# Kernel optimization log

Hardware: AMD Instinct MI355X
Metric: run time of the kernel (lower is better)

Reference implementation:

```python
import jax, jax.numpy as jnp
import numpy as np

HIDDEN = 1024
HEADS = 16
HEAD_DIM = HIDDEN // HEADS
RANK = 256
B, S = 4, 2048


def setup_inputs() -> dict:
    key = jax.random.key(0)
    ks = jax.random.split(key, 10)
    sc_in = 1.0 / np.sqrt(HIDDEN)
    sc_r = 1.0 / np.sqrt(RANK)
    inp = {"hidden_states": jax.random.normal(ks[0], (B, S, HIDDEN), dtype=jnp.float32)}
    names = ["q", "k", "v"]
    for i, n in enumerate(names):
        inp[f"{n}A"] = jax.random.normal(ks[1 + 3 * i], (HIDDEN, RANK), dtype=jnp.float32) * sc_in
        inp[f"{n}B"] = jax.random.normal(ks[2 + 3 * i], (RANK, HIDDEN), dtype=jnp.float32) * sc_r
        inp[f"{n}b"] = jnp.zeros((HIDDEN,), dtype=jnp.float32)
    return inp


def _split_heads(x):
    # [B,S,H*D] -> [B,H,S,D]
    Bh, Sh, _ = x.shape
    return x.reshape(Bh, Sh, HEADS, HEAD_DIM).transpose(0, 2, 1, 3)


def reference(hidden_states, qA, qB, qb, kA, kB, kb, vA, vB, vb):
    # Low-rank projections: x @ A @ B + b (factorized linear)
    q = hidden_states @ qA @ qB + qb
    k = hidden_states @ kA @ kB + kb
    v = hidden_states @ vA @ vB + vb
    q = _split_heads(q)  # [B,H,S,D]
    k = _split_heads(k)
    v = _split_heads(v)
    scores = jnp.einsum("bhqd,bhkd->bhqk", q, k) / np.sqrt(HEAD_DIM)
    probs = jax.nn.softmax(scores, axis=-1)  # dropout is identity at inference
    ctx = jnp.einsum("bhqk,bhkd->bhqd", probs, v)
    ctx = ctx.transpose(0, 2, 1, 3).reshape(hidden_states.shape[0], hidden_states.shape[1], HIDDEN)
    return ctx
```

## Files before the change

kernel.cpp:

```cpp
#include <hip/hip_runtime.h>


typedef unsigned short u16;
typedef unsigned int   u32;
typedef __attribute__((ext_vector_type(4)))  float    f32x4;
typedef __attribute__((ext_vector_type(16))) float    f32x16;
typedef __attribute__((ext_vector_type(8)))  short    short8;
typedef __attribute__((ext_vector_type(8)))  _Float16 half8;
typedef __attribute__((ext_vector_type(4)))  u16      u16x4;

#define HID 1024
#define R_  256
#define S_  2048
#define B_  4
#define H_  16
#define D_  64
#define M_  (B_ * S_)

#define BM 128
#define BN 64
#define BK 64

#define KVB 64
#define NT  (S_ / KVB)
#define SCL 0.18033688011112f
#define MSHIFT 8.0f

__device__ __forceinline__ u16 f2h(float f) {
    _Float16 h = (_Float16)f;
    return __builtin_bit_cast(u16, h);
}
__device__ __forceinline__ u32 pkrtz(float a, float b) {
    auto r = __builtin_amdgcn_cvt_pkrtz(a, b);
    return __builtin_bit_cast(u32, r);
}

__device__ __forceinline__ f32x4 mfma16(short8 a, short8 b, f32x4 c) {
    return __builtin_amdgcn_mfma_f32_16x16x32_f16(
        __builtin_bit_cast(half8, a), __builtin_bit_cast(half8, b), c, 0, 0, 0);
}
__device__ __forceinline__ f32x16 mfma32(short8 a, short8 b, f32x16 c) {
    return __builtin_amdgcn_mfma_f32_32x32x16_f16(
        __builtin_bit_cast(half8, a), __builtin_bit_cast(half8, b), c, 0, 0, 0);
}

__device__ __forceinline__ void gload16(const u16* g, u16* l) {
    __builtin_amdgcn_global_load_lds(
        (__attribute__((address_space(1))) const void*)g,
        (__attribute__((address_space(3))) void*)l,
        16, 0, 0);
}

#if defined(__has_builtin)
#if __has_builtin(__builtin_amdgcn_permlane32_swap)
#define HAVE_PLSWAP 1
#endif
#endif
__device__ __forceinline__ void plswap(u32 x, u32 y, u32& lo, u32& hi) {
#ifdef HAVE_PLSWAP
    typedef __attribute__((ext_vector_type(2))) unsigned uv2;
    uv2 r = __builtin_amdgcn_permlane32_swap(x, y, false, false);
    lo = r.x; hi = r.y;
#else
    u32 ty = (u32)__shfl_xor((int)y, 32);
    u32 tx = (u32)__shfl_xor((int)x, 32);
    int h = (threadIdx.x & 63) >> 5;
    lo = h ? ty : x;
    hi = h ? y : tx;
#endif
}

__global__ __launch_bounds__(256) void prep_kernel(
    const float* __restrict__ hs, u16* __restrict__ hsb,
    const float* __restrict__ qA, const float* __restrict__ kA, const float* __restrict__ vA,
    const float* __restrict__ qB, const float* __restrict__ kB, const float* __restrict__ vB,
    u16* __restrict__ At, u16* __restrict__ Bt) {
    int bx = blockIdx.x;
    if (bx < 8192) {
        int i = (bx * 256 + threadIdx.x) * 4;
        float4 v = *(const float4*)(hs + i);
        u16x4 u;
        u[0] = f2h(v.x); u[1] = f2h(v.y); u[2] = f2h(v.z); u[3] = f2h(v.w);
        *(u16x4*)(hsb + i) = u;
        return;
    }
    int pb = bx - 8192;
    int which = pb >> 10;
    int o = (pb & 1023) * 256 + threadIdx.x;
    if (which < 3) {
        const float* src = (which == 0) ? qA : (which == 1) ? kA : vA;
        u16* dst = At + (size_t)which * R_ * HID;
        int c = o >> 10, r = o & 1023;
        dst[o] = f2h(src[(size_t)r * R_ + c]);
    } else {
        int w = which - 3;
        const float* src = (w == 0) ? qB : (w == 1) ? kB : vB;
        float scl = (w == 0) ? SCL : 1.0f;
        u16* dst = Bt + (size_t)w * HID * R_;
        int c = o >> 8, r = o & 255;
        dst[o] = f2h(src[(size_t)r * HID + c] * scl);
    }
}

template <int KDIM, int NOUT, bool QKV_OUT>
__global__ __launch_bounds__(256, 3) void gemm_kernel(
    const u16* __restrict__ X, const u16* __restrict__ Wt, u16* __restrict__ Y,
    u16* __restrict__ Yv,
    const float* __restrict__ bq, const float* __restrict__ bk, const float* __restrict__ bv) {
    const int w  = blockIdx.z;
    const int m0 = blockIdx.x * BM;
    const int n0 = blockIdx.y * BN;
    const u16* Xp = X + (QKV_OUT ? (size_t)w * M_ * KDIM : (size_t)0);
    const u16* Wp = Wt + (size_t)w * NOUT * KDIM;
    u16* Yp = Y + (size_t)w * M_ * NOUT;
    const float* bias = nullptr;
    float bscl = 1.0f;
    if constexpr (QKV_OUT) { bias = (w == 0) ? bq : (w == 1) ? bk : bv; bscl = (w == 0) ? SCL : 1.0f; }

    __shared__ __align__(16) u16 As[2][BM * BK];
    __shared__ __align__(16) u16 Bs[2][BN * BK];

    const int tid  = threadIdx.x;
    const int lane = tid & 63, wv = tid >> 6;
    const int l16 = lane & 15, lg = lane >> 4;
    const int wrow = (wv >> 1) * 64, wcol = (wv & 1) * 32;

    const int sr = lane >> 3, sp = lane & 7, sc = sp ^ sr;

#define G_STAGE(bf, k0)                                                       \
    {                                                                         \
        _Pragma("unroll")                                                     \
        for (int j = 0; j < 4; ++j) {                                         \
            int ra = wv * 32 + j * 8;                                         \
            gload16(Xp + (size_t)(m0 + ra + sr) * KDIM + (k0) + sc * 8,       \
                    &As[bf][ra * 64]);                                        \
        }                                                                     \
        _Pragma("unroll")                                                     \
        for (int j = 0; j < 2; ++j) {                                         \
            int rb = wv * 16 + j * 8;                                         \
            gload16(Wp + (size_t)(n0 + rb + sr) * KDIM + (k0) + sc * 8,       \
                    &Bs[bf][rb * 64]);                                        \
        }                                                                     \
    }

    f32x4 acc[4][2];
#pragma unroll
    for (int i = 0; i < 4; ++i)
#pragma unroll
        for (int j = 0; j < 2; ++j) acc[i][j] = (f32x4){0.f, 0.f, 0.f, 0.f};

    G_STAGE(0, 0);
    int cur = 0;
    for (int k0 = 0; k0 < KDIM; k0 += BK) {
        __syncthreads();
        if (k0 + BK < KDIM) G_STAGE(cur ^ 1, k0 + BK);
        const u16* ab = &As[cur][0];
        const u16* bb = &Bs[cur][0];
#pragma unroll
        for (int ks = 0; ks < 2; ++ks) {
            short8 af[4], bf[2];
#pragma unroll
            for (int ri = 0; ri < 4; ++ri) {
                int r = wrow + ri * 16 + l16;
                int c = ks * 4 + lg;
                af[ri] = *(const short8*)(ab + r * 64 + ((c ^ (r & 7)) * 8));
            }
#pragma unroll
            for (int ci = 0; ci < 2; ++ci) {
                int r = wcol + ci * 16 + l16;
                int c = ks * 4 + lg;
                bf[ci] = *(const short8*)(bb + r * 64 + ((c ^ (r & 7)) * 8));
            }
#pragma unroll
            for (int ri = 0; ri < 4; ++ri)
#pragma unroll
                for (int ci = 0; ci < 2; ++ci)
                    acc[ri][ci] = mfma16(af[ri], bf[ci], acc[ri][ci]);
        }
        cur ^= 1;
    }
#undef G_STAGE

    if constexpr (QKV_OUT) {
        if (w == 2) {
            const int bq_ = m0 >> 11;
            const int s_base = (m0 & 2047) + wrow + lg * 4;
#pragma unroll
            for (int ci = 0; ci < 2; ++ci) {
                int c = n0 + wcol + ci * 16 + l16;
                int h = c >> 6, d = c & 63;
                u16* colp = Yv + (((size_t)(bq_ * 16 + h) * 64 + d) << 11);
                float bi = bias[c];
#pragma unroll
                for (int ri = 0; ri < 4; ++ri)
#pragma unroll
                    for (int i = 0; i < 4; ++i)
                        colp[s_base + ri * 16 + i] = f2h(acc[ri][ci][i] + bi);
            }
            return;
        }
    }
#pragma unroll
    for (int ri = 0; ri < 4; ++ri)
#pragma unroll
        for (int ci = 0; ci < 2; ++ci)
#pragma unroll
            for (int i = 0; i < 4; ++i) {
                int r = m0 + wrow + ri * 16 + lg * 4 + i;
                int c = n0 + wcol + ci * 16 + l16;
                float val = acc[ri][ci][i];
                if constexpr (QKV_OUT) val += bias[c] * bscl;
                Yp[(size_t)r * NOUT + c] = f2h(val);
            }
}

__global__ __launch_bounds__(256) void attn_kernel(
    const u16* __restrict__ Q, const u16* __restrict__ K,
    const u16* __restrict__ VT, float* __restrict__ out) {
    const int f = blockIdx.x;
    const int xcd = f & 7, idx = f >> 3;
    const int bh = xcd * 8 + (idx >> 4);
    const int qt = idx & 15;
    const int b = bh >> 4, h = bh & 15;
    const int tid = threadIdx.x, lane = tid & 63, wv = tid >> 6;
    const int l31 = lane & 31, hi = lane >> 5;
    const int q0 = qt * 128 + wv * 32;
    const int rx = l31 & 7;

    __shared__ __align__(16) u16 Ks[2][KVB * 64];
    __shared__ __align__(16) u16 Vs[2][KVB * 64];

    short8 qf[4];
    {
        const u16* qp = Q + ((size_t)(b * S_ + q0 + l31)) * HID + h * D_ + 8 * hi;
#pragma unroll
        for (int ks = 0; ks < 4; ++ks) qf[ks] = *(const short8*)(qp + 16 * ks);
    }

    f32x16 ctx0, ctx1;
#pragma unroll
    for (int i = 0; i < 16; ++i) { ctx0[i] = 0.f; ctx1[i] = 0.f; }
    float la0 = 0.f, la1 = 0.f, la2 = 0.f, la3 = 0.f;

    const int r0p = tid >> 3, pos0 = tid & 7;
    const int rA = r0p, rB = r0p + 32;
    const int slA = pos0 ^ (rA & 7), slB = pos0 ^ (rB & 7);
    const size_t kofA = (size_t)rA * HID + slA * 8, kofB = (size_t)rB * HID + slB * 8;
    const size_t vofA = (size_t)rA * S_ + slA * 8,  vofB = (size_t)rB * S_ + slB * 8;
    const int wofA = rA * 64 + pos0 * 8, wofB = rB * 64 + pos0 * 8;

    const u16* Kcur = K + (size_t)(b * S_) * HID + h * D_;
    const u16* Vcur = VT + (size_t)bh * D_ * S_;

    short8 kst0, kst1, vst0, vst1;
    kst0 = *(const short8*)(Kcur + kofA);
    kst1 = *(const short8*)(Kcur + kofB);
    vst0 = *(const short8*)(Vcur + vofA);
    vst1 = *(const short8*)(Vcur + vofB);
    *(short8*)&Ks[0][wofA] = kst0;
    *(short8*)&Ks[0][wofB] = kst1;
    *(short8*)&Vs[0][wofA] = vst0;
    *(short8*)&Vs[0][wofB] = vst1;
    __syncthreads();

    for (int t = 0; t < NT; ++t) {
        const int buf = t & 1;
        if (t + 1 < NT) {
            const u16* Kn = Kcur + (size_t)(t + 1) * KVB * HID;
            const u16* Vn = Vcur + (size_t)(t + 1) * KVB;
            kst0 = *(const short8*)(Kn + kofA);
            kst1 = *(const short8*)(Kn + kofB);
            vst0 = *(const short8*)(Vn + vofA);
            vst1 = *(const short8*)(Vn + vofB);
        }

        f32x16 p0, p1;
#pragma unroll
        for (int i = 0; i < 16; ++i) { p0[i] = -MSHIFT; p1[i] = -MSHIFT; }
        const u16* kb = &Ks[buf][0];
#pragma unroll
        for (int ks = 0; ks < 4; ++ks) {
            int sl = (2 * ks + hi) ^ rx;
            short8 a0 = *(const short8*)(kb + l31 * 64 + sl * 8);
            short8 a1 = *(const short8*)(kb + (32 + l31) * 64 + sl * 8);
            p0 = mfma32(a0, qf[ks], p0);
            p1 = mfma32(a1, qf[ks], p1);
        }

#pragma unroll
        for (int i = 0; i < 16; ++i) {
            p0[i] = __builtin_amdgcn_exp2f(p0[i]);
            p1[i] = __builtin_amdgcn_exp2f(p1[i]);
        }
#pragma unroll
        for (int i = 0; i < 4; ++i) {
            la0 += p0[i] + p0[4 + i];
            la1 += p0[8 + i] + p0[12 + i];
            la2 += p1[i] + p1[4 + i];
            la3 += p1[8 + i] + p1[12 + i];
        }

        short8 pa[4];
#define PACK_CHUNK(pv, base, dst)                                   \
        {                                                           \
            u32 x0 = pkrtz(pv[base + 0], pv[base + 1]);             \
            u32 x1 = pkrtz(pv[base + 2], pv[base + 3]);             \
            u32 x2 = pkrtz(pv[base + 4], pv[base + 5]);             \
            u32 x3 = pkrtz(pv[base + 6], pv[base + 7]);             \
            u32 w0, w1, w2, w3;                                     \
            plswap(x0, x2, w0, w2);                                 \
            plswap(x1, x3, w1, w3);                                 \
            union { u32 w[4]; short8 v; } uu;                       \
            uu.w[0] = w0; uu.w[1] = w1; uu.w[2] = w2; uu.w[3] = w3; \
            dst = uu.v;                                             \
        }
        PACK_CHUNK(p0, 0, pa[0]);
        PACK_CHUNK(p0, 8, pa[1]);
        PACK_CHUNK(p1, 0, pa[2]);
        PACK_CHUNK(p1, 8, pa[3]);
#undef PACK_CHUNK

        const u16* vb = &Vs[buf][0];
#pragma unroll
        for (int c = 0; c < 4; ++c) {
            int sl = (2 * c + hi) ^ rx;
            short8 v0 = *(const short8*)(vb + l31 * 64 + sl * 8);
            short8 v1 = *(const short8*)(vb + (32 + l31) * 64 + sl * 8);
            ctx0 = mfma32(v0, pa[c], ctx0);
            ctx1 = mfma32(v1, pa[c], ctx1);
        }

        __syncthreads();
        if (t + 1 < NT) {
            const int nb = 1 - buf;
            *(short8*)&Ks[nb][wofA] = kst0;
            *(short8*)&Ks[nb][wofB] = kst1;
            *(short8*)&Vs[nb][wofA] = vst0;
            *(short8*)&Vs[nb][wofB] = vst1;
        }
        __syncthreads();
    }

    float l = (la0 + la1) + (la2 + la3);
    l += __shfl_xor(l, 32);
    float invl = 1.0f / l;
    float* op = out + ((size_t)(b * S_ + q0 + l31)) * HID + h * D_;
#pragma unroll
    for (int g = 0; g < 4; ++g) {
        f32x4 o0, o1;
#pragma unroll
        for (int i = 0; i < 4; ++i) {
            o0[i] = ctx0[4 * g + i] * invl;
            o1[i] = ctx1[4 * g + i] * invl;
        }
        *(f32x4*)(op + 8 * g + 4 * hi) = o0;
        *(f32x4*)(op + 32 + 8 * g + 4 * hi) = o1;
    }
}

extern "C" void kernel_launch(void* const* d_in, const int* in_sizes, int n_in,
                              void* d_out, int out_size, void* d_ws, size_t ws_size,
                              hipStream_t stream) {
    const float* hs = (const float*)d_in[0];
    const float* qA = (const float*)d_in[1];
    const float* qB = (const float*)d_in[2];
    const float* qb = (const float*)d_in[3];
    const float* kA = (const float*)d_in[4];
    const float* kB = (const float*)d_in[5];
    const float* kb = (const float*)d_in[6];
    const float* vA = (const float*)d_in[7];
    const float* vB = (const float*)d_in[8];
    const float* vb = (const float*)d_in[9];

    char* ws = (char*)d_ws;
    size_t off = 0;
    u16* hsb = (u16*)(ws + off); off += (size_t)M_ * HID * 2;
    u16* At  = (u16*)(ws + off); off += (size_t)3 * R_ * HID * 2;
    u16* Bt  = (u16*)(ws + off); off += (size_t)3 * HID * R_ * 2;
    u16* T   = (u16*)(ws + off); off += (size_t)3 * M_ * R_ * 2;
    u16* QKV = (u16*)(ws + off); off += (size_t)3 * M_ * HID * 2;
    u16* VT  = (u16*)(ws + off);

    prep_kernel<<<dim3(8192 + 6144), 256, 0, stream>>>(hs, hsb, qA, kA, vA, qB, kB, vB, At, Bt);

    gemm_kernel<HID, R_, false><<<dim3(M_ / BM, R_ / BN, 3), 256, 0, stream>>>(
        hsb, At, T, nullptr, nullptr, nullptr, nullptr);
    gemm_kernel<R_, HID, true><<<dim3(M_ / BM, HID / BN, 3), 256, 0, stream>>>(
        T, Bt, QKV, VT, qb, kb, vb);

    attn_kernel<<<dim3(1024), 256, 0, stream>>>(
        QKV, QKV + (size_t)M_ * HID, VT, (float*)d_out);
}
```

Measured before the change: 150.7 us.

## Process 64 query rows per wave in attention to double K/V tile reuse

Each attention wave now handles two 32-row query sub-blocks instead of one, so every K and V fragment loaded from shared memory feeds twice as many MFMAs. The block covers 256 queries and the grid is halved to 512 blocks, which halves total K/V global and LDS traffic per query. The score accumulator is seeded from a preinitialised register vector, and launch bounds are raised to request two blocks per CU. The cost is higher register pressure from four context and four score accumulators, and fewer blocks to spread across the device.

```diff
diff --git a/kernel.cpp b/kernel.cpp
--- a/kernel.cpp
+++ b/kernel.cpp
@@ -214,33 +214,43 @@
             }
 }
 
-__global__ __launch_bounds__(256) void attn_kernel(
+__global__ __launch_bounds__(256, 2) void attn_kernel(
     const u16* __restrict__ Q, const u16* __restrict__ K,
     const u16* __restrict__ VT, float* __restrict__ out) {
     const int f = blockIdx.x;
     const int xcd = f & 7, idx = f >> 3;
-    const int bh = xcd * 8 + (idx >> 4);
-    const int qt = idx & 15;
+    const int bh = xcd * 8 + (idx >> 3);
+    const int qt = idx & 7;
     const int b = bh >> 4, h = bh & 15;
     const int tid = threadIdx.x, lane = tid & 63, wv = tid >> 6;
     const int l31 = lane & 31, hi = lane >> 5;
-    const int q0 = qt * 128 + wv * 32;
+    const int q0 = qt * 256 + wv * 64;
     const int rx = l31 & 7;
 
     __shared__ __align__(16) u16 Ks[2][KVB * 64];
     __shared__ __align__(16) u16 Vs[2][KVB * 64];
 
-    short8 qf[4];
+    short8 qf0[4], qf1[4];
     {
         const u16* qp = Q + ((size_t)(b * S_ + q0 + l31)) * HID + h * D_ + 8 * hi;
-#pragma unroll
-        for (int ks = 0; ks < 4; ++ks) qf[ks] = *(const short8*)(qp + 16 * ks);
-    }
-
-    f32x16 ctx0, ctx1;
-#pragma unroll
-    for (int i = 0; i < 16; ++i) { ctx0[i] = 0.f; ctx1[i] = 0.f; }
+        const u16* qp1 = qp + 32 * HID;
+#pragma unroll
+        for (int ks = 0; ks < 4; ++ks) {
+            qf0[ks] = *(const short8*)(qp + 16 * ks);
+            qf1[ks] = *(const short8*)(qp1 + 16 * ks);
+        }
+    }
+
+    f32x16 ctx00, ctx01, ctx10, ctx11;
+#pragma unroll
+    for (int i = 0; i < 16; ++i) { ctx00[i] = 0.f; ctx01[i] = 0.f; ctx10[i] = 0.f; ctx11[i] = 0.f; }
     float la0 = 0.f, la1 = 0.f, la2 = 0.f, la3 = 0.f;
+    float lb0 = 0.f, lb1 = 0.f, lb2 = 0.f, lb3 = 0.f;
+
+    f32x16 minit;
+#pragma unroll
+    for (int i = 0; i < 16; ++i) minit[i] = -MSHIFT;
+    asm volatile("" : "+v"(minit));
 
     const int r0p = tid >> 3, pos0 = tid & 7;
     const int rA = r0p, rB = r0p + 32;
@@ -274,33 +284,46 @@
             vst1 = *(const short8*)(Vn + vofB);
         }
 
-        f32x16 p0, p1;
-#pragma unroll
-        for (int i = 0; i < 16; ++i) { p0[i] = -MSHIFT; p1[i] = -MSHIFT; }
+        f32x16 p00, p01, p10, p11;
         const u16* kb = &Ks[buf][0];
 #pragma unroll
         for (int ks = 0; ks < 4; ++ks) {
             int sl = (2 * ks + hi) ^ rx;
             short8 a0 = *(const short8*)(kb + l31 * 64 + sl * 8);
             short8 a1 = *(const short8*)(kb + (32 + l31) * 64 + sl * 8);
-            p0 = mfma32(a0, qf[ks], p0);
-            p1 = mfma32(a1, qf[ks], p1);
+            if (ks == 0) {
+                p00 = mfma32(a0, qf0[0], minit);
+                p01 = mfma32(a1, qf0[0], minit);
+                p10 = mfma32(a0, qf1[0], minit);
+                p11 = mfma32(a1, qf1[0], minit);
+            } else {
+                p00 = mfma32(a0, qf0[ks], p00);
+                p01 = mfma32(a1, qf0[ks], p01);
+                p10 = mfma32(a0, qf1[ks], p10);
+                p11 = mfma32(a1, qf1[ks], p11);
+            }
         }
 
 #pragma unroll
         for (int i = 0; i < 16; ++i) {
-            p0[i] = __builtin_amdgcn_exp2f(p0[i]);
-            p1[i] = __builtin_amdgcn_exp2f(p1[i]);
+            p00[i] = __builtin_amdgcn_exp2f(p00[i]);
+            p01[i] = __builtin_amdgcn_exp2f(p01[i]);
+            p10[i] = __builtin_amdgcn_exp2f(p10[i]);
+            p11[i] = __builtin_amdgcn_exp2f(p11[i]);
         }
 #pragma unroll
         for (int i = 0; i < 4; ++i) {
-            la0 += p0[i] + p0[4 + i];
-            la1 += p0[8 + i] + p0[12 + i];
-            la2 += p1[i] + p1[4 + i];
-            la3 += p1[8 + i] + p1[12 + i];
-        }
-
-        short8 pa[4];
+            la0 += p00[i] + p00[4 + i];
+            la1 += p00[8 + i] + p00[12 + i];
+            la2 += p01[i] + p01[4 + i];
+            la3 += p01[8 + i] + p01[12 + i];
+            lb0 += p10[i] + p10[4 + i];
+            lb1 += p10[8 + i] + p10[12 + i];
+            lb2 += p11[i] + p11[4 + i];
+            lb3 += p11[8 + i] + p11[12 + i];
+        }
+
+        short8 pa0[4], pa1[4];
 #define PACK_CHUNK(pv, base, dst)                                   \
         {                                                           \
             u32 x0 = pkrtz(pv[base + 0], pv[base + 1]);             \
@@ -314,10 +337,14 @@
             uu.w[0] = w0; uu.w[1] = w1; uu.w[2] = w2; uu.w[3] = w3; \
             dst = uu.v;                                             \
         }
-        PACK_CHUNK(p0, 0, pa[0]);
-        PACK_CHUNK(p0, 8, pa[1]);
-        PACK_CHUNK(p1, 0, pa[2]);
-        PACK_CHUNK(p1, 8, pa[3]);
+        PACK_CHUNK(p00, 0, pa0[0]);
+        PACK_CHUNK(p00, 8, pa0[1]);
+        PACK_CHUNK(p01, 0, pa0[2]);
+        PACK_CHUNK(p01, 8, pa0[3]);
+        PACK_CHUNK(p10, 0, pa1[0]);
+        PACK_CHUNK(p10, 8, pa1[1]);
+        PACK_CHUNK(p11, 0, pa1[2]);
+        PACK_CHUNK(p11, 8, pa1[3]);
 #undef PACK_CHUNK
 
         const u16* vb = &Vs[buf][0];
@@ -326,8 +353,10 @@
             int sl = (2 * c + hi) ^ rx;
             short8 v0 = *(const short8*)(vb + l31 * 64 + sl * 8);
             short8 v1 = *(const short8*)(vb + (32 + l31) * 64 + sl * 8);
-            ctx0 = mfma32(v0, pa[c], ctx0);
-            ctx1 = mfma32(v1, pa[c], ctx1);
+            ctx00 = mfma32(v0, pa0[c], ctx00);
+            ctx01 = mfma32(v1, pa0[c], ctx01);
+            ctx10 = mfma32(v0, pa1[c], ctx10);
+            ctx11 = mfma32(v1, pa1[c], ctx11);
         }
 
         __syncthreads();
@@ -341,20 +370,27 @@
         __syncthreads();
     }
 
-    float l = (la0 + la1) + (la2 + la3);
-    l += __shfl_xor(l, 32);
-    float invl = 1.0f / l;
-    float* op = out + ((size_t)(b * S_ + q0 + l31)) * HID + h * D_;
+    float l0 = (la0 + la1) + (la2 + la3);
+    l0 += __shfl_xor(l0, 32);
+    float l1 = (lb0 + lb1) + (lb2 + lb3);
+    l1 += __shfl_xor(l1, 32);
+    float invl0 = 1.0f / l0, invl1 = 1.0f / l1;
+    float* op0 = out + ((size_t)(b * S_ + q0 + l31)) * HID + h * D_;
+    float* op1 = op0 + (size_t)32 * HID;
 #pragma unroll
     for (int g = 0; g < 4; ++g) {
-        f32x4 o0, o1;
+        f32x4 o00, o01, o10, o11;
 #pragma unroll
         for (int i = 0; i < 4; ++i) {
-            o0[i] = ctx0[4 * g + i] * invl;
-            o1[i] = ctx1[4 * g + i] * invl;
-        }
-        *(f32x4*)(op + 8 * g + 4 * hi) = o0;
-        *(f32x4*)(op + 32 + 8 * g + 4 * hi) = o1;
+            o00[i] = ctx00[4 * g + i] * invl0;
+            o01[i] = ctx01[4 * g + i] * invl0;
+            o10[i] = ctx10[4 * g + i] * invl1;
+            o11[i] = ctx11[4 * g + i] * invl1;
+        }
+        *(f32x4*)(op0 + 8 * g + 4 * hi) = o00;
+        *(f32x4*)(op0 + 32 + 8 * g + 4 * hi) = o01;
+        *(f32x4*)(op1 + 8 * g + 4 * hi) = o10;
+        *(f32x4*)(op1 + 32 + 8 * g + 4 * hi) = o11;
     }
 }
 
@@ -388,6 +424,6 @@
     gemm_kernel<R_, HID, true><<<dim3(M_ / BM, HID / BN, 3), 256, 0, stream>>>(
         T, Bt, QKV, VT, qb, kb, vb);
 
-    attn_kernel<<<dim3(1024), 256, 0, stream>>>(
+    attn_kernel<<<dim3(512), 256, 0, stream>>>(
         QKV, QKV + (size_t)M_ * HID, VT, (float*)d_out);
 }
```

Measured after the change: 143.4 us, median of 3. 4.8% less time.
